# Kernel tuning notes

Measured on AMD Instinct MI355X. Metric: run time of the kernel, lower is better.

## Reference

```python
import jax, jax.numpy as jnp
import numpy as np

BN_EPS = 1e-5

def _gin_conv(x, src, dst, w1, b1, g, bt, mu, var, w2, b2):
    # GINConv, eps=0: h = MLP(x + sum_{j in N(i)} x_j)
    n = x.shape[0]
    agg = jax.ops.segment_sum(x[src], dst, num_segments=n)  # [N, d]
    h = x + agg
    h = h @ w1 + b1
    # BatchNorm1d (eval mode, running stats)
    h = (h - mu) * jax.lax.rsqrt(var + BN_EPS) * g + bt
    h = jax.nn.elu(h)
    h = h @ w2 + b2
    return jax.nn.elu(h)

def setup_inputs() -> dict:
    key = jax.random.key(0)
    N, E, D_IN, H, OUT = 40000, 600000, 128, 128, 64
    ks = jax.random.split(key, 40)
    ki = iter(range(40))
    inp = {}
    inp['x'] = jax.random.normal(ks[next(ki)], (N, D_IN), dtype=jnp.float32)
    inp['edge_index'] = jax.random.randint(ks[next(ki)], (2, E), 0, N, dtype=jnp.int64)
    def lin(k, fin, fout):
        k1, k2 = jax.random.split(k)
        w = jax.random.normal(k1, (fin, fout), dtype=jnp.float32) / np.sqrt(fin)
        b = jax.random.normal(k2, (fout,), dtype=jnp.float32) * 0.01
        return w, b
    for i, fin in zip((1, 2, 3), (D_IN, H, H)):
        w1, b1 = lin(ks[next(ki)], fin, H)
        w2, b2 = lin(ks[next(ki)], H, H)
        g = 1.0 + 0.1 * jax.random.normal(ks[next(ki)], (H,), dtype=jnp.float32)
        bt = 0.1 * jax.random.normal(ks[next(ki)], (H,), dtype=jnp.float32)
        mu = 0.1 * jax.random.normal(ks[next(ki)], (H,), dtype=jnp.float32)
        var = jax.random.uniform(ks[next(ki)], (H,), dtype=jnp.float32, minval=0.5, maxval=1.5)
        inp.update({f'c{i}_w1': w1, f'c{i}_b1': b1, f'c{i}_g': g, f'c{i}_bt': bt,
                    f'c{i}_mu': mu, f'c{i}_var': var, f'c{i}_w2': w2, f'c{i}_b2': b2})
    inp['lin1_w'], inp['lin1_b'] = lin(ks[next(ki)], H, H)
    inp['lin2_w'], inp['lin2_b'] = lin(ks[next(ki)], H, OUT)
    return inp

def reference(x, edge_index,
              c1_w1, c1_b1, c1_g, c1_bt, c1_mu, c1_var, c1_w2, c1_b2,
              c2_w1, c2_b1, c2_g, c2_bt, c2_mu, c2_var, c2_w2, c2_b2,
              c3_w1, c3_b1, c3_g, c3_bt, c3_mu, c3_var, c3_w2, c3_b2,
              lin1_w, lin1_b, lin2_w, lin2_b):
    src, dst = edge_index[0], edge_index[1]
    h = _gin_conv(x, src, dst, c1_w1, c1_b1, c1_g, c1_bt, c1_mu, c1_var, c1_w2, c1_b2)
    h = _gin_conv(h, src, dst, c2_w1, c2_b1, c2_g, c2_bt, c2_mu, c2_var, c2_w2, c2_b2)
    h = _gin_conv(h, src, dst, c3_w1, c3_b1, c3_g, c3_bt, c3_mu, c3_var, c3_w2, c3_b2)
    h = jax.nn.elu(h @ lin1_w + lin1_b)
    # dropout p=0.5 is identity in eval mode
    return h @ lin2_w + lin2_b
```

## Files before the change

### kernel.cpp

```cpp
#include <hip/hip_runtime.h>
#include <cmath>

#define NODES 40000
#define EDGES 600000
#define HD    128
#define CAP   80
#define BN_EPS 1e-5f

typedef short bf16x8 __attribute__((ext_vector_type(8)));
typedef float f32x4  __attribute__((ext_vector_type(4)));
typedef unsigned short u16;
typedef unsigned int   u32;

__device__ __forceinline__ float bf2f(u16 u) {
  union { u32 i; float f; } v; v.i = ((u32)u) << 16; return v.f;
}
__device__ __forceinline__ u16 f2bf(float f) {
  union { float f; u32 i; } v; v.f = f;
  u32 r = v.i + 0x7FFF + ((v.i >> 16) & 1);
  return (u16)(r >> 16);
}
__device__ __forceinline__ float elu(float x) {
  return x > 0.f ? x : __expf(x) - 1.f;
}

struct WPrep { const float* s[8]; u16* d[8]; };

__global__ __launch_bounds__(256) void prep_all(const float4* __restrict__ x4,
                                                ushort4* __restrict__ xb4,
                                                WPrep p, int* __restrict__ cnt) {
  const int bid = blockIdx.x;
  const int tid = threadIdx.x;
  if (bid < 5000) {
    int i = bid * 256 + tid;
    float4 v = x4[i];
    ushort4 o;
    o.x = f2bf(v.x); o.y = f2bf(v.y); o.z = f2bf(v.z); o.w = f2bf(v.w);
    xb4[i] = o;
  } else if (bid < 5128) {
    int b = bid - 5000;
    int m = b >> 4, xx = b & 15;
    int N = (m == 7) ? 64 : 128;
    int tiles_n = N / 32;
    int tx = xx % tiles_n, tk = xx / tiles_n;
    if (tk >= 4) return;
    __shared__ float t[32][33];
    int c = tid & 31, r8 = tid >> 5;
    const float* s = p.s[m];
    for (int rr = 0; rr < 32; rr += 8)
      t[rr + r8][c] = s[(size_t)(tk * 32 + rr + r8) * N + tx * 32 + c];
    __syncthreads();
    u16* d = p.d[m];
    for (int rr = 0; rr < 32; rr += 8)
      d[(size_t)(tx * 32 + rr + r8) * HD + tk * 32 + c] = f2bf(t[c][rr + r8]);
  } else {
    int i = (bid - 5128) * 256 + tid;
    if (i < NODES) cnt[i] = 0;
  }
}

__global__ __launch_bounds__(256) void bucket_fill(const int* __restrict__ ei,
                                                   int* __restrict__ cnt,
                                                   int* __restrict__ bucket) {
  int e = blockIdx.x * 256 + threadIdx.x;
  if (e >= EDGES) return;
  int s = ei[e];
  int d = ei[EDGES + e];
  int pos = atomicAdd(&cnt[d], 1);
  if (pos < CAP) bucket[d * CAP + pos] = s;
}

__global__ __launch_bounds__(256) void gather_w(const u16* __restrict__ x,
                                                const int* __restrict__ cnt,
                                                const int* __restrict__ bucket,
                                                u16* __restrict__ agg) {
  const int tid = threadIdx.x;
  const int half = (tid >> 5) & 1;
  const int hl = tid & 31;
  const int node = blockIdx.x * 8 + (tid >> 6) * 2 + half;
  const int i0 = node * CAP;

  uint2 self = ((const uint2*)(x + (size_t)node * HD))[hl];
  int sv = bucket[i0 + hl];
  int deg = cnt[node];
  if (deg > CAP) deg = CAP;

  float a0 = bf2f((u16)self.x), a1 = bf2f((u16)(self.x >> 16));
  float a2 = bf2f((u16)self.y), a3 = bf2f((u16)(self.y >> 16));

  for (int c0 = 0; c0 < deg; c0 += 32) {
    int m = deg - c0;
    if (m > 32) m = 32;
    for (int j = 0; j < m; j += 8) {
      int idx[8];
      uint2 uu[8];
#pragma unroll
      for (int jj = 0; jj < 8; ++jj) {
        int src = j + jj < m ? j + jj : 0;
        idx[jj] = __shfl(sv, src, 32);
      }
#pragma unroll
      for (int jj = 0; jj < 8; ++jj)
        uu[jj] = ((const uint2*)(x + (size_t)idx[jj] * HD))[hl];
#pragma unroll
      for (int jj = 0; jj < 8; ++jj) {
        if (j + jj < m) {
          a0 += bf2f((u16)uu[jj].x);
          a1 += bf2f((u16)(uu[jj].x >> 16));
          a2 += bf2f((u16)uu[jj].y);
          a3 += bf2f((u16)(uu[jj].y >> 16));
        }
      }
    }
    int nc = c0 + 32;
    if (nc < deg) {
      int a = nc + hl;
      sv = bucket[i0 + (a < CAP ? a : 0)];
    }
  }
  uint2 pk;
  pk.x = (u32)f2bf(a0) | ((u32)f2bf(a1) << 16);
  pk.y = (u32)f2bf(a2) | ((u32)f2bf(a3) << 16);
  ((uint2*)(agg + (size_t)node * HD))[hl] = pk;
}

__global__ __launch_bounds__(256) void mlp_fused(
    const u16* __restrict__ A, const u16* __restrict__ W1t,
    const float* __restrict__ b1, const float* __restrict__ g,
    const float* __restrict__ bt, const float* __restrict__ mu,
    const float* __restrict__ vr, const u16* __restrict__ W2t,
    const float* __restrict__ b2, u16* __restrict__ out) {
  constexpr int PK = HD + 8;
  __shared__ u16 L[192][PK];

  const int tid = threadIdx.x;
  const int wv = tid >> 6, lane = tid & 63;
  const int col = lane & 15, kg = lane >> 4;

#pragma unroll
  for (int t = tid; t < 128 * 16; t += 256) {
    int r = t >> 4, c8 = t & 15;
    *(bf16x8*)&L[r][c8 * 8] = *(const bf16x8*)(W1t + (size_t)r * HD + c8 * 8);
  }
  __syncthreads();

  const int strip = blockIdx.x * 4 + wv;
  const u16* Arow = A + (size_t)(strip * 16 + col) * HD;
  const int hrow = 128 + wv * 16;

  f32x4 acc[8];
#pragma unroll
  for (int t = 0; t < 8; ++t) acc[t] = (f32x4){0.f, 0.f, 0.f, 0.f};
#pragma unroll
  for (int kk = 0; kk < HD; kk += 32) {
    bf16x8 av = *(const bf16x8*)(Arow + kk + kg * 8);
#pragma unroll
    for (int t = 0; t < 8; ++t) {
      bf16x8 bv = *(const bf16x8*)&L[t * 16 + col][kk + kg * 8];
      acc[t] = __builtin_amdgcn_mfma_f32_16x16x32_bf16(av, bv, acc[t], 0, 0, 0);
    }
  }
  __syncthreads();

#pragma unroll
  for (int t = tid; t < 128 * 16; t += 256) {
    int r = t >> 4, c8 = t & 15;
    *(bf16x8*)&L[r][c8 * 8] = *(const bf16x8*)(W2t + (size_t)r * HD + c8 * 8);
  }
#pragma unroll
  for (int t = 0; t < 8; ++t) {
    int c = t * 16 + col;
    float rs = rsqrtf(vr[c] + BN_EPS) * g[c];
    float bb = bt[c] + (b1[c] - mu[c]) * rs;
#pragma unroll
    for (int r = 0; r < 4; ++r)
      L[hrow + kg * 4 + r][c] = f2bf(elu(acc[t][r] * rs + bb));
  }
  __syncthreads();

  f32x4 acc2[8];
#pragma unroll
  for (int t = 0; t < 8; ++t) acc2[t] = (f32x4){0.f, 0.f, 0.f, 0.f};
#pragma unroll
  for (int kk = 0; kk < HD; kk += 32) {
    bf16x8 av = *(const bf16x8*)&L[hrow + col][kk + kg * 8];
#pragma unroll
    for (int t = 0; t < 8; ++t) {
      bf16x8 bv = *(const bf16x8*)&L[t * 16 + col][kk + kg * 8];
      acc2[t] = __builtin_amdgcn_mfma_f32_16x16x32_bf16(av, bv, acc2[t], 0, 0, 0);
    }
  }
#pragma unroll
  for (int t = 0; t < 8; ++t) {
    int c = t * 16 + col;
    float bb = b2[c];
#pragma unroll
    for (int r = 0; r < 4; ++r)
      L[hrow + kg * 4 + r][c] = f2bf(elu(acc2[t][r] + bb));
  }
  {
    int r0 = lane >> 4, seg = lane & 15;
#pragma unroll
    for (int rr = 0; rr < 16; rr += 4) {
      int row = rr + r0;
      *(float4*)((char*)(out + (size_t)(strip * 16 + row) * HD) + seg * 16) =
          *(const float4*)((const char*)&L[hrow + row][0] + seg * 16);
    }
  }
}

__global__ __launch_bounds__(256) void mlp3_head(
    const u16* __restrict__ A, const u16* __restrict__ W1t,
    const float* __restrict__ b1, const float* __restrict__ g,
    const float* __restrict__ bt, const float* __restrict__ mu,
    const float* __restrict__ vr, const u16* __restrict__ W2t,
    const float* __restrict__ b2, const u16* __restrict__ L1t,
    const float* __restrict__ lb1, const u16* __restrict__ L2t,
    const float* __restrict__ lb2, float* __restrict__ out) {
  constexpr int PK = HD + 8;
  __shared__ u16 L[192][PK];

  const int tid = threadIdx.x;
  const int wv = tid >> 6, lane = tid & 63;
  const int col = lane & 15, kg = lane >> 4;

#pragma unroll
  for (int t = tid; t < 128 * 16; t += 256) {
    int r = t >> 4, c8 = t & 15;
    *(bf16x8*)&L[r][c8 * 8] = *(const bf16x8*)(W1t + (size_t)r * HD + c8 * 8);
  }
  __syncthreads();

  const int strip = blockIdx.x * 4 + wv;
  const u16* Arow = A + (size_t)(strip * 16 + col) * HD;
  const int hrow = 128 + wv * 16;

  f32x4 acc[8];
#pragma unroll
  for (int t = 0; t < 8; ++t) acc[t] = (f32x4){0.f, 0.f, 0.f, 0.f};
#pragma unroll
  for (int kk = 0; kk < HD; kk += 32) {
    bf16x8 av = *(const bf16x8*)(Arow + kk + kg * 8);
#pragma unroll
    for (int t = 0; t < 8; ++t) {
      bf16x8 bv = *(const bf16x8*)&L[t * 16 + col][kk + kg * 8];
      acc[t] = __builtin_amdgcn_mfma_f32_16x16x32_bf16(av, bv, acc[t], 0, 0, 0);
    }
  }
  __syncthreads();
#pragma unroll
  for (int t = tid; t < 128 * 16; t += 256) {
    int r = t >> 4, c8 = t & 15;
    *(bf16x8*)&L[r][c8 * 8] = *(const bf16x8*)(W2t + (size_t)r * HD + c8 * 8);
  }
#pragma unroll
  for (int t = 0; t < 8; ++t) {
    int c = t * 16 + col;
    float rs = rsqrtf(vr[c] + BN_EPS) * g[c];
    float bb = bt[c] + (b1[c] - mu[c]) * rs;
#pragma unroll
    for (int r = 0; r < 4; ++r)
      L[hrow + kg * 4 + r][c] = f2bf(elu(acc[t][r] * rs + bb));
  }
  __syncthreads();

#pragma unroll
  for (int t = 0; t < 8; ++t) acc[t] = (f32x4){0.f, 0.f, 0.f, 0.f};
#pragma unroll
  for (int kk = 0; kk < HD; kk += 32) {
    bf16x8 av = *(const bf16x8*)&L[hrow + col][kk + kg * 8];
#pragma unroll
    for (int t = 0; t < 8; ++t) {
      bf16x8 bv = *(const bf16x8*)&L[t * 16 + col][kk + kg * 8];
      acc[t] = __builtin_amdgcn_mfma_f32_16x16x32_bf16(av, bv, acc[t], 0, 0, 0);
    }
  }
  __syncthreads();
#pragma unroll
  for (int t = tid; t < 128 * 16; t += 256) {
    int r = t >> 4, c8 = t & 15;
    *(bf16x8*)&L[r][c8 * 8] = *(const bf16x8*)(L1t + (size_t)r * HD + c8 * 8);
  }
#pragma unroll
  for (int t = 0; t < 8; ++t) {
    int c = t * 16 + col;
    float bb = b2[c];
#pragma unroll
    for (int r = 0; r < 4; ++r)
      L[hrow + kg * 4 + r][c] = f2bf(elu(acc[t][r] + bb));
  }
  __syncthreads();

#pragma unroll
  for (int t = 0; t < 8; ++t) acc[t] = (f32x4){0.f, 0.f, 0.f, 0.f};
#pragma unroll
  for (int kk = 0; kk < HD; kk += 32) {
    bf16x8 av = *(const bf16x8*)&L[hrow + col][kk + kg * 8];
#pragma unroll
    for (int t = 0; t < 8; ++t) {
      bf16x8 bv = *(const bf16x8*)&L[t * 16 + col][kk + kg * 8];
      acc[t] = __builtin_amdgcn_mfma_f32_16x16x32_bf16(av, bv, acc[t], 0, 0, 0);
    }
  }
  __syncthreads();
#pragma unroll
  for (int t = tid; t < 64 * 16; t += 256) {
    int r = t >> 4, c8 = t & 15;
    *(bf16x8*)&L[r][c8 * 8] = *(const bf16x8*)(L2t + (size_t)r * HD + c8 * 8);
  }
#pragma unroll
  for (int t = 0; t < 8; ++t) {
    int c = t * 16 + col;
    float bb = lb1[c];
#pragma unroll
    for (int r = 0; r < 4; ++r)
      L[hrow + kg * 4 + r][c] = f2bf(elu(acc[t][r] + bb));
  }
  __syncthreads();

  f32x4 acc2[4];
#pragma unroll
  for (int t = 0; t < 4; ++t) acc2[t] = (f32x4){0.f, 0.f, 0.f, 0.f};
#pragma unroll
  for (int kk = 0; kk < HD; kk += 32) {
    bf16x8 av = *(const bf16x8*)&L[hrow + col][kk + kg * 8];
#pragma unroll
    for (int t = 0; t < 4; ++t) {
      bf16x8 bv = *(const bf16x8*)&L[t * 16 + col][kk + kg * 8];
      acc2[t] = __builtin_amdgcn_mfma_f32_16x16x32_bf16(av, bv, acc2[t], 0, 0, 0);
    }
  }
#pragma unroll
  for (int t = 0; t < 4; ++t) {
    int c = t * 16 + col;
    float bb = lb2[c];
#pragma unroll
    for (int r = 0; r < 4; ++r)
      ((float*)&L[hrow + kg * 4 + r][0])[c] = acc2[t][r] + bb;
  }
  {
    int r0 = lane >> 4, seg = lane & 15;
#pragma unroll
    for (int rr = 0; rr < 16; rr += 4) {
      int row = rr + r0;
      *(float4*)((char*)(out + (size_t)(strip * 16 + row) * 64) + seg * 16) =
          *(const float4*)((const char*)&L[hrow + row][0] + seg * 16);
    }
  }
}

extern "C" void kernel_launch(void* const* d_in, const int* in_sizes, int n_in,
                              void* d_out, int out_size, void* d_ws, size_t ws_size,
                              hipStream_t stream) {
  const float* x = (const float*)d_in[0];
  const int* ei  = (const int*)d_in[1];
  const float* p[30];
  for (int i = 0; i < 30 && i < n_in; ++i) p[i] = (const float*)d_in[i];

  const size_t FEAT = (size_t)NODES * HD;
  u16* xb   = (u16*)d_ws;
  u16* tmp  = xb + FEAT;
  u16* wt   = tmp + FEAT;
  u16* wts[8];
  for (int m = 0; m < 8; ++m) wts[m] = wt + (size_t)m * HD * HD;
  int* cnt    = (int*)(wt + 8 * HD * HD);
  int* bucket = cnt + NODES;

  dim3 blk(256);
  const int edgeGrid = (EDGES + 255) / 256;
  const int gathGrid = NODES / 8;
  const int gemmGrid = NODES / 64;

  WPrep wp;
  const int widx[8] = {2, 8, 10, 16, 18, 24, 26, 28};
  for (int m = 0; m < 8; ++m) { wp.s[m] = p[widx[m]]; wp.d[m] = wts[m]; }
  prep_all<<<5285, blk, 0, stream>>>((const float4*)x, (ushort4*)xb, wp, cnt);
  bucket_fill<<<edgeGrid, blk, 0, stream>>>(ei, cnt, bucket);

  for (int l = 0; l < 2; ++l) {
    const int base = 2 + l * 8;
    gather_w<<<gathGrid, blk, 0, stream>>>(xb, cnt, bucket, tmp);
    mlp_fused<<<gemmGrid, blk, 0, stream>>>(
        tmp, wts[l * 2], p[base + 1], p[base + 2], p[base + 3], p[base + 4],
        p[base + 5], wts[l * 2 + 1], p[base + 7], xb);
  }
  gather_w<<<gathGrid, blk, 0, stream>>>(xb, cnt, bucket, tmp);
  mlp3_head<<<gemmGrid, blk, 0, stream>>>(
      tmp, wts[4], p[19], p[20], p[21], p[22], p[23], wts[5], p[25],
      wts[6], p[27], wts[7], p[29], (float*)d_out);
}
```

Before: 265.2 us.

## Fuse neighbor gather into GIN MLP kernels with ping-pong feature buffers

Moves the neighbor aggregation into the MLP kernels: each wave gathers its 16 node rows directly into shared memory, then runs the MFMA GEMMs on them. This removes the separate gather launches and the global write and reread of the aggregated features per layer. Features alternate between two buffers so that no layer overwrites its own input. The cost is far fewer waves for the latency-bound gather, since each wave now serially processes 16 nodes, which may reduce memory-level parallelism.

```diff
diff --git a/kernel.cpp b/kernel.cpp
--- a/kernel.cpp
+++ b/kernel.cpp
@@ -6,6 +6,7 @@
 #define HD    128
 #define CAP   80
 #define BN_EPS 1e-5f
+#define PK    (HD + 8)
 
 typedef short bf16x8 __attribute__((ext_vector_type(8)));
 typedef float f32x4  __attribute__((ext_vector_type(4)));
@@ -70,90 +71,89 @@
   if (pos < CAP) bucket[d * CAP + pos] = s;
 }
 
-__global__ __launch_bounds__(256) void gather_w(const u16* __restrict__ x,
-                                                const int* __restrict__ cnt,
-                                                const int* __restrict__ bucket,
-                                                u16* __restrict__ agg) {
-  const int tid = threadIdx.x;
-  const int half = (tid >> 5) & 1;
-  const int hl = tid & 31;
-  const int node = blockIdx.x * 8 + (tid >> 6) * 2 + half;
-  const int i0 = node * CAP;
-
-  uint2 self = ((const uint2*)(x + (size_t)node * HD))[hl];
-  int sv = bucket[i0 + hl];
-  int deg = cnt[node];
-  if (deg > CAP) deg = CAP;
-
-  float a0 = bf2f((u16)self.x), a1 = bf2f((u16)(self.x >> 16));
-  float a2 = bf2f((u16)self.y), a3 = bf2f((u16)(self.y >> 16));
-
-  for (int c0 = 0; c0 < deg; c0 += 32) {
-    int m = deg - c0;
-    if (m > 32) m = 32;
-    for (int j = 0; j < m; j += 8) {
-      int idx[8];
-      uint2 uu[8];
-#pragma unroll
-      for (int jj = 0; jj < 8; ++jj) {
-        int src = j + jj < m ? j + jj : 0;
-        idx[jj] = __shfl(sv, src, 32);
-      }
-#pragma unroll
-      for (int jj = 0; jj < 8; ++jj)
-        uu[jj] = ((const uint2*)(x + (size_t)idx[jj] * HD))[hl];
-#pragma unroll
-      for (int jj = 0; jj < 8; ++jj) {
-        if (j + jj < m) {
-          a0 += bf2f((u16)uu[jj].x);
-          a1 += bf2f((u16)(uu[jj].x >> 16));
-          a2 += bf2f((u16)uu[jj].y);
-          a3 += bf2f((u16)(uu[jj].y >> 16));
+__device__ __forceinline__ void gather16(const u16* __restrict__ x,
+                                         const int* __restrict__ cnt,
+                                         const int* __restrict__ bucket,
+                                         int strip16, int lane,
+                                         u16* __restrict__ Lbase) {
+  const int half = lane >> 5;
+  const int hl = lane & 31;
+  for (int r = 0; r < 8; ++r) {
+    const int nrow = r * 2 + half;
+    const int node = strip16 + nrow;
+    const int i0 = node * CAP;
+    uint2 self = ((const uint2*)(x + (size_t)node * HD))[hl];
+    int sv = bucket[i0 + hl];
+    int deg = cnt[node];
+    if (deg > CAP) deg = CAP;
+    float a0 = bf2f((u16)self.x), a1 = bf2f((u16)(self.x >> 16));
+    float a2 = bf2f((u16)self.y), a3 = bf2f((u16)(self.y >> 16));
+    for (int c0 = 0; c0 < deg; c0 += 32) {
+      int m = deg - c0;
+      if (m > 32) m = 32;
+      for (int j = 0; j < m; j += 8) {
+        int idx[8];
+        uint2 uu[8];
+#pragma unroll
+        for (int jj = 0; jj < 8; ++jj) {
+          int src = j + jj < m ? j + jj : 0;
+          idx[jj] = __shfl(sv, src, 32);
+        }
+#pragma unroll
+        for (int jj = 0; jj < 8; ++jj)
+          uu[jj] = ((const uint2*)(x + (size_t)idx[jj] * HD))[hl];
+#pragma unroll
+        for (int jj = 0; jj < 8; ++jj) {
+          if (j + jj < m) {
+            a0 += bf2f((u16)uu[jj].x);
+            a1 += bf2f((u16)(uu[jj].x >> 16));
+            a2 += bf2f((u16)uu[jj].y);
+            a3 += bf2f((u16)(uu[jj].y >> 16));
+          }
         }
       }
-    }
-    int nc = c0 + 32;
-    if (nc < deg) {
-      int a = nc + hl;
-      sv = bucket[i0 + (a < CAP ? a : 0)];
-    }
-  }
-  uint2 pk;
-  pk.x = (u32)f2bf(a0) | ((u32)f2bf(a1) << 16);
-  pk.y = (u32)f2bf(a2) | ((u32)f2bf(a3) << 16);
-  ((uint2*)(agg + (size_t)node * HD))[hl] = pk;
-}
-
-__global__ __launch_bounds__(256) void mlp_fused(
-    const u16* __restrict__ A, const u16* __restrict__ W1t,
+      int nc = c0 + 32;
+      if (nc < deg) {
+        int a = nc + hl;
+        sv = bucket[i0 + (a < CAP ? a : 0)];
+      }
+    }
+    uint2 pk;
+    pk.x = (u32)f2bf(a0) | ((u32)f2bf(a1) << 16);
+    pk.y = (u32)f2bf(a2) | ((u32)f2bf(a3) << 16);
+    *(uint2*)(Lbase + (size_t)nrow * PK + hl * 4) = pk;
+  }
+}
+
+__global__ __launch_bounds__(256) void gin_layer(
+    const u16* __restrict__ xin, const int* __restrict__ cnt,
+    const int* __restrict__ bucket, const u16* __restrict__ W1t,
     const float* __restrict__ b1, const float* __restrict__ g,
     const float* __restrict__ bt, const float* __restrict__ mu,
     const float* __restrict__ vr, const u16* __restrict__ W2t,
-    const float* __restrict__ b2, u16* __restrict__ out) {
-  constexpr int PK = HD + 8;
+    const float* __restrict__ b2, u16* __restrict__ xout) {
   __shared__ u16 L[192][PK];
 
   const int tid = threadIdx.x;
   const int wv = tid >> 6, lane = tid & 63;
   const int col = lane & 15, kg = lane >> 4;
+  const int strip = blockIdx.x * 4 + wv;
+  const int hrow = 128 + wv * 16;
 
 #pragma unroll
   for (int t = tid; t < 128 * 16; t += 256) {
     int r = t >> 4, c8 = t & 15;
     *(bf16x8*)&L[r][c8 * 8] = *(const bf16x8*)(W1t + (size_t)r * HD + c8 * 8);
   }
-  __syncthreads();
-
-  const int strip = blockIdx.x * 4 + wv;
-  const u16* Arow = A + (size_t)(strip * 16 + col) * HD;
-  const int hrow = 128 + wv * 16;
+  gather16(xin, cnt, bucket, strip * 16, lane, &L[hrow][0]);
+  __syncthreads();
 
   f32x4 acc[8];
 #pragma unroll
   for (int t = 0; t < 8; ++t) acc[t] = (f32x4){0.f, 0.f, 0.f, 0.f};
 #pragma unroll
   for (int kk = 0; kk < HD; kk += 32) {
-    bf16x8 av = *(const bf16x8*)(Arow + kk + kg * 8);
+    bf16x8 av = *(const bf16x8*)&L[hrow + col][kk + kg * 8];
 #pragma unroll
     for (int t = 0; t < 8; ++t) {
       bf16x8 bv = *(const bf16x8*)&L[t * 16 + col][kk + kg * 8];
@@ -203,44 +203,43 @@
 #pragma unroll
     for (int rr = 0; rr < 16; rr += 4) {
       int row = rr + r0;
-      *(float4*)((char*)(out + (size_t)(strip * 16 + row) * HD) + seg * 16) =
+      *(float4*)((char*)(xout + (size_t)(strip * 16 + row) * HD) + seg * 16) =
           *(const float4*)((const char*)&L[hrow + row][0] + seg * 16);
     }
   }
 }
 
-__global__ __launch_bounds__(256) void mlp3_head(
-    const u16* __restrict__ A, const u16* __restrict__ W1t,
+__global__ __launch_bounds__(256) void gin_layer3_head(
+    const u16* __restrict__ xin, const int* __restrict__ cnt,
+    const int* __restrict__ bucket, const u16* __restrict__ W1t,
     const float* __restrict__ b1, const float* __restrict__ g,
     const float* __restrict__ bt, const float* __restrict__ mu,
     const float* __restrict__ vr, const u16* __restrict__ W2t,
     const float* __restrict__ b2, const u16* __restrict__ L1t,
     const float* __restrict__ lb1, const u16* __restrict__ L2t,
     const float* __restrict__ lb2, float* __restrict__ out) {
-  constexpr int PK = HD + 8;
   __shared__ u16 L[192][PK];
 
   const int tid = threadIdx.x;
   const int wv = tid >> 6, lane = tid & 63;
   const int col = lane & 15, kg = lane >> 4;
+  const int strip = blockIdx.x * 4 + wv;
+  const int hrow = 128 + wv * 16;
 
 #pragma unroll
   for (int t = tid; t < 128 * 16; t += 256) {
     int r = t >> 4, c8 = t & 15;
     *(bf16x8*)&L[r][c8 * 8] = *(const bf16x8*)(W1t + (size_t)r * HD + c8 * 8);
   }
-  __syncthreads();
-
-  const int strip = blockIdx.x * 4 + wv;
-  const u16* Arow = A + (size_t)(strip * 16 + col) * HD;
-  const int hrow = 128 + wv * 16;
+  gather16(xin, cnt, bucket, strip * 16, lane, &L[hrow][0]);
+  __syncthreads();
 
   f32x4 acc[8];
 #pragma unroll
   for (int t = 0; t < 8; ++t) acc[t] = (f32x4){0.f, 0.f, 0.f, 0.f};
 #pragma unroll
   for (int kk = 0; kk < HD; kk += 32) {
-    bf16x8 av = *(const bf16x8*)(Arow + kk + kg * 8);
+    bf16x8 av = *(const bf16x8*)&L[hrow + col][kk + kg * 8];
 #pragma unroll
     for (int t = 0; t < 8; ++t) {
       bf16x8 bv = *(const bf16x8*)&L[t * 16 + col][kk + kg * 8];
@@ -358,9 +357,9 @@
   for (int i = 0; i < 30 && i < n_in; ++i) p[i] = (const float*)d_in[i];
 
   const size_t FEAT = (size_t)NODES * HD;
-  u16* xb   = (u16*)d_ws;
-  u16* tmp  = xb + FEAT;
-  u16* wt   = tmp + FEAT;
+  u16* xb0  = (u16*)d_ws;
+  u16* xb1  = xb0 + FEAT;
+  u16* wt   = xb1 + FEAT;
   u16* wts[8];
   for (int m = 0; m < 8; ++m) wts[m] = wt + (size_t)m * HD * HD;
   int* cnt    = (int*)(wt + 8 * HD * HD);
@@ -368,24 +367,19 @@
 
   dim3 blk(256);
   const int edgeGrid = (EDGES + 255) / 256;
-  const int gathGrid = NODES / 8;
   const int gemmGrid = NODES / 64;
 
   WPrep wp;
   const int widx[8] = {2, 8, 10, 16, 18, 24, 26, 28};
   for (int m = 0; m < 8; ++m) { wp.s[m] = p[widx[m]]; wp.d[m] = wts[m]; }
-  prep_all<<<5285, blk, 0, stream>>>((const float4*)x, (ushort4*)xb, wp, cnt);
+  prep_all<<<5285, blk, 0, stream>>>((const float4*)x, (ushort4*)xb0, wp, cnt);
   bucket_fill<<<edgeGrid, blk, 0, stream>>>(ei, cnt, bucket);
 
-  for (int l = 0; l < 2; ++l) {
-    const int base = 2 + l * 8;
-    gather_w<<<gathGrid, blk, 0, stream>>>(xb, cnt, bucket, tmp);
-    mlp_fused<<<gemmGrid, blk, 0, stream>>>(
-        tmp, wts[l * 2], p[base + 1], p[base + 2], p[base + 3], p[base + 4],
-        p[base + 5], wts[l * 2 + 1], p[base + 7], xb);
-  }
-  gather_w<<<gathGrid, blk, 0, stream>>>(xb, cnt, bucket, tmp);
-  mlp3_head<<<gemmGrid, blk, 0, stream>>>(
-      tmp, wts[4], p[19], p[20], p[21], p[22], p[23], wts[5], p[25],
+  gin_layer<<<gemmGrid, blk, 0, stream>>>(
+      xb0, cnt, bucket, wts[0], p[3], p[4], p[5], p[6], p[7], wts[1], p[9], xb1);
+  gin_layer<<<gemmGrid, blk, 0, stream>>>(
+      xb1, cnt, bucket, wts[2], p[11], p[12], p[13], p[14], p[15], wts[3], p[17], xb0);
+  gin_layer3_head<<<gemmGrid, blk, 0, stream>>>(
+      xb0, cnt, bucket, wts[4], p[19], p[20], p[21], p[22], p[23], wts[5], p[25],
       wts[6], p[27], wts[7], p[29], (float*)d_out);
 }
```

Measured after the change: 276.3 us. +4.2%, slower.

## Fuse all GIN stages into one persistent cooperative kernel with grid syncs

Applied to the files above, without the earlier changes.

Replaces the sequence of eight launches (prep, bucket fill, three gathers, three MLPs) with one cooperative persistent kernel of 256 blocks × 1024 threads. Stages are separated by grid.sync, and work is grid-strided so each half-wave handles several nodes and each block handles 10 GEMM strips. Feature buffers are padded to 40960 rows so the strip mapping covers the whole range; only the final output write is guarded. The aim is to remove launch gaps and tail effects between stages. In exchange it adds grid-wide barriers and lower occupancy (one large block per CU, only 10 of 16 waves active in GEMM phases), which may slow the latency-bound gather. The original multi-kernel path is kept as a fallback.

```diff
diff --git a/kernel.cpp b/kernel.cpp
--- a/kernel.cpp
+++ b/kernel.cpp
@@ -1,11 +1,19 @@
 #include <hip/hip_runtime.h>
+#include <hip/hip_cooperative_groups.h>
 #include <cmath>
 
+namespace cg = cooperative_groups;
+
 #define NODES 40000
+#define NPAD  40960
 #define EDGES 600000
 #define HD    128
 #define CAP   80
 #define BN_EPS 1e-5f
+#define PK    (HD + 8)
+#define GRID  256
+#define BLK   1024
+#define SPB   10
 
 typedef short bf16x8 __attribute__((ext_vector_type(8)));
 typedef float f32x4  __attribute__((ext_vector_type(4)));
@@ -22,6 +30,363 @@
 }
 __device__ __forceinline__ float elu(float x) {
   return x > 0.f ? x : __expf(x) - 1.f;
+}
+
+struct Params {
+  const float* x; const int* ei;
+  const float* ws[8]; u16* wd[8];
+  const float* b1[3]; const float* gg[3]; const float* bt[3];
+  const float* mu[3]; const float* vr[3]; const float* b2[3];
+  const float* lb1; const float* lb2;
+  u16* xb; u16* tmp; int* cnt; int* bucket; float* out;
+};
+
+__device__ __forceinline__ void gather_phase(const u16* __restrict__ x,
+                                             const int* __restrict__ cnt,
+                                             const int* __restrict__ bucket,
+                                             u16* __restrict__ agg,
+                                             int hw, int nhw) {
+  const int hl = threadIdx.x & 31;
+  for (int node = hw; node < NODES; node += nhw) {
+    const int i0 = node * CAP;
+    uint2 self = ((const uint2*)(x + (size_t)node * HD))[hl];
+    int sv = bucket[i0 + hl];
+    int deg = cnt[node];
+    if (deg > CAP) deg = CAP;
+    float a0 = bf2f((u16)self.x), a1 = bf2f((u16)(self.x >> 16));
+    float a2 = bf2f((u16)self.y), a3 = bf2f((u16)(self.y >> 16));
+    for (int c0 = 0; c0 < deg; c0 += 32) {
+      int m = deg - c0;
+      if (m > 32) m = 32;
+      for (int j = 0; j < m; j += 8) {
+        int idx[8];
+        uint2 uu[8];
+#pragma unroll
+        for (int jj = 0; jj < 8; ++jj) {
+          int src = j + jj < m ? j + jj : 0;
+          idx[jj] = __shfl(sv, src, 32);
+        }
+#pragma unroll
+        for (int jj = 0; jj < 8; ++jj)
+          uu[jj] = ((const uint2*)(x + (size_t)idx[jj] * HD))[hl];
+#pragma unroll
+        for (int jj = 0; jj < 8; ++jj) {
+          if (j + jj < m) {
+            a0 += bf2f((u16)uu[jj].x);
+            a1 += bf2f((u16)(uu[jj].x >> 16));
+            a2 += bf2f((u16)uu[jj].y);
+            a3 += bf2f((u16)(uu[jj].y >> 16));
+          }
+        }
+      }
+      int nc = c0 + 32;
+      if (nc < deg) {
+        int a = nc + hl;
+        sv = bucket[i0 + (a < CAP ? a : 0)];
+      }
+    }
+    uint2 pk;
+    pk.x = (u32)f2bf(a0) | ((u32)f2bf(a1) << 16);
+    pk.y = (u32)f2bf(a2) | ((u32)f2bf(a3) << 16);
+    ((uint2*)(agg + (size_t)node * HD))[hl] = pk;
+  }
+}
+
+__device__ __forceinline__ void mlp2_phase(u16 (*L)[PK],
+    const u16* __restrict__ A, const u16* __restrict__ W1t,
+    const float* __restrict__ b1, const float* __restrict__ g,
+    const float* __restrict__ bt, const float* __restrict__ mu,
+    const float* __restrict__ vr, const u16* __restrict__ W2t,
+    const float* __restrict__ b2, u16* __restrict__ out, int tid, int bid) {
+  const int wv = tid >> 6, lane = tid & 63;
+  const int col = lane & 15, kg = lane >> 4;
+  const bool act = (wv < SPB);
+  const int strip = bid * SPB + wv;
+  const int hrow = 128 + wv * 16;
+
+  for (int t = tid; t < 128 * 16; t += BLK) {
+    int r = t >> 4, c8 = t & 15;
+    *(bf16x8*)&L[r][c8 * 8] = *(const bf16x8*)(W1t + (size_t)r * HD + c8 * 8);
+  }
+  __syncthreads();
+
+  f32x4 acc[8];
+#pragma unroll
+  for (int t = 0; t < 8; ++t) acc[t] = (f32x4){0.f, 0.f, 0.f, 0.f};
+  if (act) {
+    const u16* Arow = A + (size_t)(strip * 16 + col) * HD;
+#pragma unroll
+    for (int kk = 0; kk < HD; kk += 32) {
+      bf16x8 av = *(const bf16x8*)(Arow + kk + kg * 8);
+#pragma unroll
+      for (int t = 0; t < 8; ++t) {
+        bf16x8 bv = *(const bf16x8*)&L[t * 16 + col][kk + kg * 8];
+        acc[t] = __builtin_amdgcn_mfma_f32_16x16x32_bf16(av, bv, acc[t], 0, 0, 0);
+      }
+    }
+  }
+  __syncthreads();
+
+  for (int t = tid; t < 128 * 16; t += BLK) {
+    int r = t >> 4, c8 = t & 15;
+    *(bf16x8*)&L[r][c8 * 8] = *(const bf16x8*)(W2t + (size_t)r * HD + c8 * 8);
+  }
+  if (act) {
+#pragma unroll
+    for (int t = 0; t < 8; ++t) {
+      int c = t * 16 + col;
+      float rs = rsqrtf(vr[c] + BN_EPS) * g[c];
+      float bb = bt[c] + (b1[c] - mu[c]) * rs;
+#pragma unroll
+      for (int r = 0; r < 4; ++r)
+        L[hrow + kg * 4 + r][c] = f2bf(elu(acc[t][r] * rs + bb));
+    }
+  }
+  __syncthreads();
+
+  f32x4 acc2[8];
+#pragma unroll
+  for (int t = 0; t < 8; ++t) acc2[t] = (f32x4){0.f, 0.f, 0.f, 0.f};
+  if (act) {
+#pragma unroll
+    for (int kk = 0; kk < HD; kk += 32) {
+      bf16x8 av = *(const bf16x8*)&L[hrow + col][kk + kg * 8];
+#pragma unroll
+      for (int t = 0; t < 8; ++t) {
+        bf16x8 bv = *(const bf16x8*)&L[t * 16 + col][kk + kg * 8];
+        acc2[t] = __builtin_amdgcn_mfma_f32_16x16x32_bf16(av, bv, acc2[t], 0, 0, 0);
+      }
+    }
+#pragma unroll
+    for (int t = 0; t < 8; ++t) {
+      int c = t * 16 + col;
+      float bb = b2[c];
+#pragma unroll
+      for (int r = 0; r < 4; ++r)
+        L[hrow + kg * 4 + r][c] = f2bf(elu(acc2[t][r] + bb));
+    }
+    int r0 = lane >> 4, seg = lane & 15;
+#pragma unroll
+    for (int rr = 0; rr < 16; rr += 4) {
+      int row = rr + r0;
+      *(float4*)((char*)(out + (size_t)(strip * 16 + row) * HD) + seg * 16) =
+          *(const float4*)((const char*)&L[hrow + row][0] + seg * 16);
+    }
+  }
+}
+
+__device__ __forceinline__ void head_phase(u16 (*L)[PK],
+    const u16* __restrict__ A, const u16* __restrict__ W1t,
+    const float* __restrict__ b1, const float* __restrict__ g,
+    const float* __restrict__ bt, const float* __restrict__ mu,
+    const float* __restrict__ vr, const u16* __restrict__ W2t,
+    const float* __restrict__ b2, const u16* __restrict__ L1t,
+    const float* __restrict__ lb1, const u16* __restrict__ L2t,
+    const float* __restrict__ lb2, float* __restrict__ out, int tid, int bid) {
+  const int wv = tid >> 6, lane = tid & 63;
+  const int col = lane & 15, kg = lane >> 4;
+  const bool act = (wv < SPB);
+  const int strip = bid * SPB + wv;
+  const int hrow = 128 + wv * 16;
+
+  for (int t = tid; t < 128 * 16; t += BLK) {
+    int r = t >> 4, c8 = t & 15;
+    *(bf16x8*)&L[r][c8 * 8] = *(const bf16x8*)(W1t + (size_t)r * HD + c8 * 8);
+  }
+  __syncthreads();
+
+  f32x4 acc[8];
+#pragma unroll
+  for (int t = 0; t < 8; ++t) acc[t] = (f32x4){0.f, 0.f, 0.f, 0.f};
+  if (act) {
+    const u16* Arow = A + (size_t)(strip * 16 + col) * HD;
+#pragma unroll
+    for (int kk = 0; kk < HD; kk += 32) {
+      bf16x8 av = *(const bf16x8*)(Arow + kk + kg * 8);
+#pragma unroll
+      for (int t = 0; t < 8; ++t) {
+        bf16x8 bv = *(const bf16x8*)&L[t * 16 + col][kk + kg * 8];
+        acc[t] = __builtin_amdgcn_mfma_f32_16x16x32_bf16(av, bv, acc[t], 0, 0, 0);
+      }
+    }
+  }
+  __syncthreads();
+  for (int t = tid; t < 128 * 16; t += BLK) {
+    int r = t >> 4, c8 = t & 15;
+    *(bf16x8*)&L[r][c8 * 8] = *(const bf16x8*)(W2t + (size_t)r * HD + c8 * 8);
+  }
+  if (act) {
+#pragma unroll
+    for (int t = 0; t < 8; ++t) {
+      int c = t * 16 + col;
+      float rs = rsqrtf(vr[c] + BN_EPS) * g[c];
+      float bb = bt[c] + (b1[c] - mu[c]) * rs;
+#pragma unroll
+      for (int r = 0; r < 4; ++r)
+        L[hrow + kg * 4 + r][c] = f2bf(elu(acc[t][r] * rs + bb));
+    }
+  }
+  __syncthreads();
+
+#pragma unroll
+  for (int t = 0; t < 8; ++t) acc[t] = (f32x4){0.f, 0.f, 0.f, 0.f};
+  if (act) {
+#pragma unroll
+    for (int kk = 0; kk < HD; kk += 32) {
+      bf16x8 av = *(const bf16x8*)&L[hrow + col][kk + kg * 8];
+#pragma unroll
+      for (int t = 0; t < 8; ++t) {
+        bf16x8 bv = *(const bf16x8*)&L[t * 16 + col][kk + kg * 8];
+        acc[t] = __builtin_amdgcn_mfma_f32_16x16x32_bf16(av, bv, acc[t], 0, 0, 0);
+      }
+    }
+  }
+  __syncthreads();
+  for (int t = tid; t < 128 * 16; t += BLK) {
+    int r = t >> 4, c8 = t & 15;
+    *(bf16x8*)&L[r][c8 * 8] = *(const bf16x8*)(L1t + (size_t)r * HD + c8 * 8);
+  }
+  if (act) {
+#pragma unroll
+    for (int t = 0; t < 8; ++t) {
+      int c = t * 16 + col;
+      float bb = b2[c];
+#pragma unroll
+      for (int r = 0; r < 4; ++r)
+        L[hrow + kg * 4 + r][c] = f2bf(elu(acc[t][r] + bb));
+    }
+  }
+  __syncthreads();
+
+#pragma unroll
+  for (int t = 0; t < 8; ++t) acc[t] = (f32x4){0.f, 0.f, 0.f, 0.f};
+  if (act) {
+#pragma unroll
+    for (int kk = 0; kk < HD; kk += 32) {
+      bf16x8 av = *(const bf16x8*)&L[hrow + col][kk + kg * 8];
+#pragma unroll
+      for (int t = 0; t < 8; ++t) {
+        bf16x8 bv = *(const bf16x8*)&L[t * 16 + col][kk + kg * 8];
+        acc[t] = __builtin_amdgcn_mfma_f32_16x16x32_bf16(av, bv, acc[t], 0, 0, 0);
+      }
+    }
+  }
+  __syncthreads();
+  for (int t = tid; t < 64 * 16; t += BLK) {
+    int r = t >> 4, c8 = t & 15;
+    *(bf16x8*)&L[r][c8 * 8] = *(const bf16x8*)(L2t + (size_t)r * HD + c8 * 8);
+  }
+  if (act) {
+#pragma unroll
+    for (int t = 0; t < 8; ++t) {
+      int c = t * 16 + col;
+      float bb = lb1[c];
+#pragma unroll
+      for (int r = 0; r < 4; ++r)
+        L[hrow + kg * 4 + r][c] = f2bf(elu(acc[t][r] + bb));
+    }
+  }
+  __syncthreads();
+
+  if (act) {
+    f32x4 acc2[4];
+#pragma unroll
+    for (int t = 0; t < 4; ++t) acc2[t] = (f32x4){0.f, 0.f, 0.f, 0.f};
+#pragma unroll
+    for (int kk = 0; kk < HD; kk += 32) {
+      bf16x8 av = *(const bf16x8*)&L[hrow + col][kk + kg * 8];
+#pragma unroll
+      for (int t = 0; t < 4; ++t) {
+        bf16x8 bv = *(const bf16x8*)&L[t * 16 + col][kk + kg * 8];
+        acc2[t] = __builtin_amdgcn_mfma_f32_16x16x32_bf16(av, bv, acc2[t], 0, 0, 0);
+      }
+    }
+#pragma unroll
+    for (int t = 0; t < 4; ++t) {
+      int c = t * 16 + col;
+      float bb = lb2[c];
+#pragma unroll
+      for (int r = 0; r < 4; ++r)
+        ((float*)&L[hrow + kg * 4 + r][0])[c] = acc2[t][r] + bb;
+    }
+    if (strip < NODES / 16) {
+      int r0 = lane >> 4, seg = lane & 15;
+#pragma unroll
+      for (int rr = 0; rr < 16; rr += 4) {
+        int row = rr + r0;
+        *(float4*)((char*)(out + (size_t)(strip * 16 + row) * 64) + seg * 16) =
+            *(const float4*)((const char*)&L[hrow + row][0] + seg * 16);
+      }
+    }
+  }
+}
+
+__global__ __launch_bounds__(BLK, 4) void gin_all(Params P) {
+  cg::grid_group grid = cg::this_grid();
+  __shared__ u16 L[288][PK];
+  const int tid = threadIdx.x, bid = blockIdx.x;
+  const int hw = (bid * BLK + tid) >> 5;
+  const int nhw = GRID * BLK / 32;
+
+  {
+    const float4* x4 = (const float4*)P.x;
+    ushort4* xb4 = (ushort4*)P.xb;
+    for (int i = bid * BLK + tid; i < NODES * HD / 4; i += GRID * BLK) {
+      float4 v = x4[i];
+      ushort4 o;
+      o.x = f2bf(v.x); o.y = f2bf(v.y); o.z = f2bf(v.z); o.w = f2bf(v.w);
+      xb4[i] = o;
+    }
+    for (int i = bid * BLK + tid; i < NODES; i += GRID * BLK) P.cnt[i] = 0;
+    if (bid < 128) {
+      int m = bid >> 4, xx = bid & 15;
+      int N = (m == 7) ? 64 : 128;
+      int tn = N / 32;
+      int tx = xx % tn, tk = xx / tn;
+      bool valid = (tk < 4);
+      float* tf = (float*)&L[0][0];
+      int c = tid & 31, r8 = tid >> 5;
+      if (valid && tid < 256) {
+        const float* s = P.ws[m];
+        for (int rr = 0; rr < 32; rr += 8)
+          tf[(rr + r8) * 33 + c] = s[(size_t)(tk * 32 + rr + r8) * N + tx * 32 + c];
+      }
+      __syncthreads();
+      if (valid && tid < 256) {
+        u16* d = P.wd[m];
+        for (int rr = 0; rr < 32; rr += 8)
+          d[(size_t)(tx * 32 + rr + r8) * HD + tk * 32 + c] = f2bf(tf[c * 33 + rr + r8]);
+      }
+    }
+  }
+  __threadfence();
+  grid.sync();
+
+  for (int e = bid * BLK + tid; e < EDGES; e += GRID * BLK) {
+    int s = P.ei[e];
+    int d = P.ei[EDGES + e];
+    int pos = atomicAdd(&P.cnt[d], 1);
+    if (pos < CAP) P.bucket[d * CAP + pos] = s;
+  }
+  __threadfence();
+  grid.sync();
+
+  for (int l = 0; l < 3; ++l) {
+    gather_phase(P.xb, P.cnt, P.bucket, P.tmp, hw, nhw);
+    __threadfence();
+    grid.sync();
+    if (l < 2)
+      mlp2_phase(L, P.tmp, P.wd[2 * l], P.b1[l], P.gg[l], P.bt[l], P.mu[l],
+                 P.vr[l], P.wd[2 * l + 1], P.b2[l], P.xb, tid, bid);
+    else
+      head_phase(L, P.tmp, P.wd[4], P.b1[2], P.gg[2], P.bt[2], P.mu[2],
+                 P.vr[2], P.wd[5], P.b2[2], P.wd[6], P.lb1, P.wd[7], P.lb2,
+                 P.out, tid, bid);
+    if (l < 2) {
+      __threadfence();
+      grid.sync();
+    }
+  }
 }
 
 struct WPrep { const float* s[8]; u16* d[8]; };
@@ -75,79 +440,28 @@
                                                 const int* __restrict__ bucket,
                                                 u16* __restrict__ agg) {
   const int tid = threadIdx.x;
-  const int half = (tid >> 5) & 1;
-  const int hl = tid & 31;
-  const int node = blockIdx.x * 8 + (tid >> 6) * 2 + half;
-  const int i0 = node * CAP;
-
-  uint2 self = ((const uint2*)(x + (size_t)node * HD))[hl];
-  int sv = bucket[i0 + hl];
-  int deg = cnt[node];
-  if (deg > CAP) deg = CAP;
-
-  float a0 = bf2f((u16)self.x), a1 = bf2f((u16)(self.x >> 16));
-  float a2 = bf2f((u16)self.y), a3 = bf2f((u16)(self.y >> 16));
-
-  for (int c0 = 0; c0 < deg; c0 += 32) {
-    int m = deg - c0;
-    if (m > 32) m = 32;
-    for (int j = 0; j < m; j += 8) {
-      int idx[8];
-      uint2 uu[8];
-#pragma unroll
-      for (int jj = 0; jj < 8; ++jj) {
-        int src = j + jj < m ? j + jj : 0;
-        idx[jj] = __shfl(sv, src, 32);
-      }
-#pragma unroll
-      for (int jj = 0; jj < 8; ++jj)
-        uu[jj] = ((const uint2*)(x + (size_t)idx[jj] * HD))[hl];
-#pragma unroll
-      for (int jj = 0; jj < 8; ++jj) {
-        if (j + jj < m) {
-          a0 += bf2f((u16)uu[jj].x);
-          a1 += bf2f((u16)(uu[jj].x >> 16));
-          a2 += bf2f((u16)uu[jj].y);
-          a3 += bf2f((u16)(uu[jj].y >> 16));
-        }
-      }
-    }
-    int nc = c0 + 32;
-    if (nc < deg) {
-      int a = nc + hl;
-      sv = bucket[i0 + (a < CAP ? a : 0)];
-    }
-  }
-  uint2 pk;
-  pk.x = (u32)f2bf(a0) | ((u32)f2bf(a1) << 16);
-  pk.y = (u32)f2bf(a2) | ((u32)f2bf(a3) << 16);
-  ((uint2*)(agg + (size_t)node * HD))[hl] = pk;
-}
-
-__global__ __launch_bounds__(256) void mlp_fused(
+  const int hw = blockIdx.x * 8 + (tid >> 5);
+  gather_phase(x, cnt, bucket, agg, hw, NODES + 8);
+}
+
+__global__ __launch_bounds__(256) void mlp_fused_k(
     const u16* __restrict__ A, const u16* __restrict__ W1t,
     const float* __restrict__ b1, const float* __restrict__ g,
     const float* __restrict__ bt, const float* __restrict__ mu,
     const float* __restrict__ vr, const u16* __restrict__ W2t,
     const float* __restrict__ b2, u16* __restrict__ out) {
-  constexpr int PK = HD + 8;
   __shared__ u16 L[192][PK];
-
   const int tid = threadIdx.x;
   const int wv = tid >> 6, lane = tid & 63;
   const int col = lane & 15, kg = lane >> 4;
-
-#pragma unroll
   for (int t = tid; t < 128 * 16; t += 256) {
     int r = t >> 4, c8 = t & 15;
     *(bf16x8*)&L[r][c8 * 8] = *(const bf16x8*)(W1t + (size_t)r * HD + c8 * 8);
   }
   __syncthreads();
-
   const int strip = blockIdx.x * 4 + wv;
   const u16* Arow = A + (size_t)(strip * 16 + col) * HD;
   const int hrow = 128 + wv * 16;
-
   f32x4 acc[8];
 #pragma unroll
   for (int t = 0; t < 8; ++t) acc[t] = (f32x4){0.f, 0.f, 0.f, 0.f};
@@ -161,8 +475,6 @@
     }
   }
   __syncthreads();
-
-#pragma unroll
   for (int t = tid; t < 128 * 16; t += 256) {
     int r = t >> 4, c8 = t & 15;
     *(bf16x8*)&L[r][c8 * 8] = *(const bf16x8*)(W2t + (size_t)r * HD + c8 * 8);
@@ -177,7 +489,6 @@
       L[hrow + kg * 4 + r][c] = f2bf(elu(acc[t][r] * rs + bb));
   }
   __syncthreads();
-
   f32x4 acc2[8];
 #pragma unroll
   for (int t = 0; t < 8; ++t) acc2[t] = (f32x4){0.f, 0.f, 0.f, 0.f};
@@ -209,7 +520,7 @@
   }
 }
 
-__global__ __launch_bounds__(256) void mlp3_head(
+__global__ __launch_bounds__(256) void mlp3_head_k(
     const u16* __restrict__ A, const u16* __restrict__ W1t,
     const float* __restrict__ b1, const float* __restrict__ g,
     const float* __restrict__ bt, const float* __restrict__ mu,
@@ -217,24 +528,18 @@
     const float* __restrict__ b2, const u16* __restrict__ L1t,
     const float* __restrict__ lb1, const u16* __restrict__ L2t,
     const float* __restrict__ lb2, float* __restrict__ out) {
-  constexpr int PK = HD + 8;
   __shared__ u16 L[192][PK];
-
   const int tid = threadIdx.x;
   const int wv = tid >> 6, lane = tid & 63;
   const int col = lane & 15, kg = lane >> 4;
-
-#pragma unroll
   for (int t = tid; t < 128 * 16; t += 256) {
     int r = t >> 4, c8 = t & 15;
     *(bf16x8*)&L[r][c8 * 8] = *(const bf16x8*)(W1t + (size_t)r * HD + c8 * 8);
   }
   __syncthreads();
-
   const int strip = blockIdx.x * 4 + wv;
   const u16* Arow = A + (size_t)(strip * 16 + col) * HD;
   const int hrow = 128 + wv * 16;
-
   f32x4 acc[8];
 #pragma unroll
   for (int t = 0; t < 8; ++t) acc[t] = (f32x4){0.f, 0.f, 0.f, 0.f};
@@ -248,7 +553,6 @@
     }
   }
   __syncthreads();
-#pragma unroll
   for (int t = tid; t < 128 * 16; t += 256) {
     int r = t >> 4, c8 = t & 15;
     *(bf16x8*)&L[r][c8 * 8] = *(const bf16x8*)(W2t + (size_t)r * HD + c8 * 8);
@@ -263,7 +567,6 @@
       L[hrow + kg * 4 + r][c] = f2bf(elu(acc[t][r] * rs + bb));
   }
   __syncthreads();
-
 #pragma unroll
   for (int t = 0; t < 8; ++t) acc[t] = (f32x4){0.f, 0.f, 0.f, 0.f};
 #pragma unroll
@@ -276,7 +579,6 @@
     }
   }
   __syncthreads();
-#pragma unroll
   for (int t = tid; t < 128 * 16; t += 256) {
     int r = t >> 4, c8 = t & 15;
     *(bf16x8*)&L[r][c8 * 8] = *(const bf16x8*)(L1t + (size_t)r * HD + c8 * 8);
@@ -290,7 +592,6 @@
       L[hrow + kg * 4 + r][c] = f2bf(elu(acc[t][r] + bb));
   }
   __syncthreads();
-
 #pragma unroll
   for (int t = 0; t < 8; ++t) acc[t] = (f32x4){0.f, 0.f, 0.f, 0.f};
 #pragma unroll
@@ -303,7 +604,6 @@
     }
   }
   __syncthreads();
-#pragma unroll
   for (int t = tid; t < 64 * 16; t += 256) {
     int r = t >> 4, c8 = t & 15;
     *(bf16x8*)&L[r][c8 * 8] = *(const bf16x8*)(L2t + (size_t)r * HD + c8 * 8);
@@ -317,7 +617,6 @@
       L[hrow + kg * 4 + r][c] = f2bf(elu(acc[t][r] + bb));
   }
   __syncthreads();
-
   f32x4 acc2[4];
 #pragma unroll
   for (int t = 0; t < 4; ++t) acc2[t] = (f32x4){0.f, 0.f, 0.f, 0.f};
@@ -352,40 +651,66 @@
 extern "C" void kernel_launch(void* const* d_in, const int* in_sizes, int n_in,
                               void* d_out, int out_size, void* d_ws, size_t ws_size,
                               hipStream_t stream) {
-  const float* x = (const float*)d_in[0];
-  const int* ei  = (const int*)d_in[1];
   const float* p[30];
   for (int i = 0; i < 30 && i < n_in; ++i) p[i] = (const float*)d_in[i];
 
-  const size_t FEAT = (size_t)NODES * HD;
-  u16* xb   = (u16*)d_ws;
-  u16* tmp  = xb + FEAT;
-  u16* wt   = tmp + FEAT;
-  u16* wts[8];
-  for (int m = 0; m < 8; ++m) wts[m] = wt + (size_t)m * HD * HD;
+  const size_t FEATP = (size_t)NPAD * HD;
+  u16* xb  = (u16*)d_ws;
+  u16* tmp = xb + FEATP;
+  u16* wt  = tmp + FEATP;
   int* cnt    = (int*)(wt + 8 * HD * HD);
   int* bucket = cnt + NODES;
+
+  Params pa;
+  pa.x = p[0];
+  pa.ei = (const int*)d_in[1];
+  const int widx[8] = {2, 8, 10, 16, 18, 24, 26, 28};
+  for (int m = 0; m < 8; ++m) {
+    pa.ws[m] = p[widx[m]];
+    pa.wd[m] = wt + (size_t)m * HD * HD;
+  }
+  for (int l = 0; l < 3; ++l) {
+    const int base = 2 + l * 8;
+    pa.b1[l] = p[base + 1]; pa.gg[l] = p[base + 2]; pa.bt[l] = p[base + 3];
+    pa.mu[l] = p[base + 4]; pa.vr[l] = p[base + 5]; pa.b2[l] = p[base + 7];
+  }
+  pa.lb1 = p[27];
+  pa.lb2 = p[29];
+  pa.xb = xb; pa.tmp = tmp; pa.cnt = cnt; pa.bucket = bucket;
+  pa.out = (float*)d_out;
+
+  static int coop_ok = -1;
+  if (coop_ok < 0) {
+    int attr = 0;
+    hipDeviceGetAttribute(&attr, hipDeviceAttributeCooperativeLaunch, 0);
+    int nb = 0;
+    hipError_t qe = hipOccupancyMaxActiveBlocksPerMultiprocessor(&nb, gin_all, BLK, 0);
+    coop_ok = (attr != 0 && qe == hipSuccess && nb >= 1) ? 1 : 0;
+  }
+  if (coop_ok) {
+    void* args[] = {&pa};
+    hipError_t le = hipLaunchCooperativeKernel((void*)gin_all, dim3(GRID),
+                                               dim3(BLK), args, 0, stream);
+    if (le == hipSuccess) return;
+    coop_ok = 0;
+  }
 
   dim3 blk(256);
   const int edgeGrid = (EDGES + 255) / 256;
   const int gathGrid = NODES / 8;
   const int gemmGrid = NODES / 64;
-
   WPrep wp;
-  const int widx[8] = {2, 8, 10, 16, 18, 24, 26, 28};
-  for (int m = 0; m < 8; ++m) { wp.s[m] = p[widx[m]]; wp.d[m] = wts[m]; }
-  prep_all<<<5285, blk, 0, stream>>>((const float4*)x, (ushort4*)xb, wp, cnt);
-  bucket_fill<<<edgeGrid, blk, 0, stream>>>(ei, cnt, bucket);
-
+  for (int m = 0; m < 8; ++m) { wp.s[m] = pa.ws[m]; wp.d[m] = pa.wd[m]; }
+  prep_all<<<5285, blk, 0, stream>>>((const float4*)pa.x, (ushort4*)xb, wp, cnt);
+  bucket_fill<<<edgeGrid, blk, 0, stream>>>(pa.ei, cnt, bucket);
   for (int l = 0; l < 2; ++l) {
-    const int base = 2 + l * 8;
     gather_w<<<gathGrid, blk, 0, stream>>>(xb, cnt, bucket, tmp);
-    mlp_fused<<<gemmGrid, blk, 0, stream>>>(
-        tmp, wts[l * 2], p[base + 1], p[base + 2], p[base + 3], p[base + 4],
-        p[base + 5], wts[l * 2 + 1], p[base + 7], xb);
+    mlp_fused_k<<<gemmGrid, blk, 0, stream>>>(
+        tmp, pa.wd[2 * l], pa.b1[l], pa.gg[l], pa.bt[l], pa.mu[l], pa.vr[l],
+        pa.wd[2 * l + 1], pa.b2[l], xb);
   }
   gather_w<<<gathGrid, blk, 0, stream>>>(xb, cnt, bucket, tmp);
-  mlp3_head<<<gemmGrid, blk, 0, stream>>>(
-      tmp, wts[4], p[19], p[20], p[21], p[22], p[23], wts[5], p[25],
-      wts[6], p[27], wts[7], p[29], (float*)d_out);
-}
+  mlp3_head_k<<<gemmGrid, blk, 0, stream>>>(
+      tmp, pa.wd[4], pa.b1[2], pa.gg[2], pa.bt[2], pa.mu[2], pa.vr[2],
+      pa.wd[5], pa.b2[2], pa.wd[6], pa.lb1, pa.wd[7], pa.lb2, pa.out);
+}
```

Result: no change. 264.4 us (-0.3%).
